# Kernel optimization log

Measured on AMD Instinct MI355X. Metric: run time of the kernel, lower is better.

The kernel has to match this reference:

```python
import jax, jax.numpy as jnp
import numpy as np

B, T, F, H, L = 128, 512, 64, 512, 2


def setup_inputs() -> dict:
    key = jax.random.key(0)
    ks = jax.random.split(key, 12)
    s = 1.0 / np.sqrt(H)
    inp = {
        "x": jax.random.normal(ks[0], (B, T, F), dtype=jnp.float32),
        "w_ih_0": jax.random.uniform(ks[1], (4 * H, F), jnp.float32, -s, s),
        "w_hh_0": jax.random.uniform(ks[2], (4 * H, H), jnp.float32, -s, s),
        "b_ih_0": jax.random.uniform(ks[3], (4 * H,), jnp.float32, -s, s),
        "b_hh_0": jax.random.uniform(ks[4], (4 * H,), jnp.float32, -s, s),
        "w_ih_1": jax.random.uniform(ks[5], (4 * H, H), jnp.float32, -s, s),
        "w_hh_1": jax.random.uniform(ks[6], (4 * H, H), jnp.float32, -s, s),
        "b_ih_1": jax.random.uniform(ks[7], (4 * H,), jnp.float32, -s, s),
        "b_hh_1": jax.random.uniform(ks[8], (4 * H,), jnp.float32, -s, s),
        "lin_w": jax.random.uniform(ks[9], (1, H), jnp.float32, -s, s),
        "lin_b": jax.random.uniform(ks[10], (1,), jnp.float32, -s, s),
    }
    return inp


def _lstm_layer(x, w_ih, w_hh, b_ih, b_hh):
    # x: [B, T, Din] -> hidden sequence [B, T, H]; PyTorch gate order i,f,g,o
    Bb = x.shape[0]
    Hh = w_hh.shape[1]
    # precompute input projections for all timesteps (big GEMM outside the scan)
    x_proj = jnp.einsum('bti,gi->btg', x, w_ih) + b_ih + b_hh  # [B, T, 4H]

    def step(carry, xt):
        h, c = carry
        gates = xt + h @ w_hh.T  # [B, 4H]
        i, f, g, o = jnp.split(gates, 4, axis=-1)
        i = jax.nn.sigmoid(i)
        f = jax.nn.sigmoid(f)
        g = jnp.tanh(g)
        o = jax.nn.sigmoid(o)
        c = f * c + i * g
        h = o * jnp.tanh(c)
        return (h, c), h

    h0 = jnp.zeros((Bb, Hh), x.dtype)
    (_, _), hs = jax.lax.scan(step, (h0, h0), jnp.swapaxes(x_proj, 0, 1))
    return jnp.swapaxes(hs, 0, 1)  # [B, T, H]


def reference(x, w_ih_0, w_hh_0, b_ih_0, b_hh_0,
              w_ih_1, w_hh_1, b_ih_1, b_hh_1, lin_w, lin_b):
    h = _lstm_layer(x, w_ih_0, w_hh_0, b_ih_0, b_hh_0)
    h = _lstm_layer(h, w_ih_1, w_hh_1, b_ih_1, b_hh_1)
    last = h[:, -1, :]           # [B, H]
    return last @ lin_w.T + lin_b  # [B, 1]
```

## Files before the change

kernel.cpp:

```cpp
#include <hip/hip_runtime.h>
#include <hip/hip_bf16.h>

typedef __bf16 bf16x8 __attribute__((ext_vector_type(8)));
typedef float f32x4 __attribute__((ext_vector_type(4)));
typedef unsigned uint4v __attribute__((ext_vector_type(4)));
typedef unsigned long long u64;

constexpr int Bb = 128, Tt = 512, Ff = 64, Hh = 512, Gg = 2048;
constexpr int K0 = Hh + Ff;
constexpr int K1 = Hh + Hh;
constexpr int NITER = Tt + 1;

constexpr size_t OFF_W0  = 0;
constexpr size_t OFF_W1  = OFF_W0 + (size_t)Gg * K0 * 2;
constexpr size_t OFF_B0  = OFF_W1 + (size_t)Gg * K1 * 2;
constexpr size_t OFF_B1  = OFF_B0 + (size_t)Gg * 4;
constexpr size_t OFF_HI0 = OFF_B1 + (size_t)Gg * 4;
constexpr size_t OFF_HI1 = OFF_HI0 + (size_t)2 * Bb * Hh * 4;
constexpr size_t OFF_HF  = OFF_HI1 + (size_t)2 * Bb * Hh * 4;
constexpr size_t OFF_FLG = OFF_HF + (size_t)Bb * Hh * 4;

__global__ void prep(const float* __restrict__ wih0, const float* __restrict__ whh0,
                     const float* __restrict__ bih0, const float* __restrict__ bhh0,
                     const float* __restrict__ wih1, const float* __restrict__ whh1,
                     const float* __restrict__ bih1, const float* __restrict__ bhh1,
                     unsigned char* __restrict__ ws)
{
  __hip_bfloat16* W0 = reinterpret_cast<__hip_bfloat16*>(ws + OFF_W0);
  __hip_bfloat16* W1 = reinterpret_cast<__hip_bfloat16*>(ws + OFF_W1);
  float* B0 = reinterpret_cast<float*>(ws + OFF_B0);
  float* B1 = reinterpret_cast<float*>(ws + OFF_B1);
  unsigned* HI0 = reinterpret_cast<unsigned*>(ws + OFF_HI0);
  unsigned* HI1 = reinterpret_cast<unsigned*>(ws + OFF_HI1);
  unsigned* FLG = reinterpret_cast<unsigned*>(ws + OFF_FLG);

  const size_t tid = (size_t)blockIdx.x * blockDim.x + threadIdx.x;
  const size_t stp = (size_t)gridDim.x * blockDim.x;

  for (size_t i = tid; i < (size_t)Gg * K0; i += stp) {
    int g = (int)(i / K0), k = (int)(i % K0);
    float v = (k < Hh) ? whh0[(size_t)g * Hh + k] : wih0[(size_t)g * Ff + (k - Hh)];
    W0[i] = __float2bfloat16(v);
  }
  for (size_t i = tid; i < (size_t)Gg * K1; i += stp) {
    int g = (int)(i / K1), k = (int)(i % K1);
    float v = (k < Hh) ? whh1[(size_t)g * Hh + k] : wih1[(size_t)g * Hh + (k - Hh)];
    W1[i] = __float2bfloat16(v);
  }
  for (size_t i = tid; i < (size_t)Gg; i += stp) {
    B0[i] = bih0[i] + bhh0[i];
    B1[i] = bih1[i] + bhh1[i];
  }
  for (size_t i = tid; i < (size_t)2 * Bb * Hh; i += stp) { HI0[i] = 0u; HI1[i] = 0u; }
  for (size_t i = tid; i < (size_t)NITER * 256; i += stp) FLG[i] = 0u;
}

__device__ __forceinline__ float sigf(float x)   { return 1.f / (1.f + __expf(-x)); }
__device__ __forceinline__ float tanhf_(float x) { return 1.f - 2.f / (1.f + __expf(2.f * x)); }

__device__ __forceinline__ unsigned pack_hl(float v) {
  __bf16 hb = (__bf16)v;
  __bf16 lb = (__bf16)(v - (float)hb);
  return (unsigned)__builtin_bit_cast(unsigned short, hb)
       | ((unsigned)__builtin_bit_cast(unsigned short, lb) << 16);
}

__device__ __forceinline__ void lds_frag(const unsigned* sh, int fr, int cb,
                                         bf16x8& hi, bf16x8& lo) {
  const int sw = (fr & 7) << 2;
  const unsigned* row = sh + fr * Hh;
  uint4v qa = *reinterpret_cast<const uint4v*>(row + (cb ^ sw));
  uint4v qb = *reinterpret_cast<const uint4v*>(row + ((cb + 4) ^ sw));
  uint4v hw = { __builtin_amdgcn_perm(qa[1], qa[0], 0x05040100u),
                __builtin_amdgcn_perm(qa[3], qa[2], 0x05040100u),
                __builtin_amdgcn_perm(qb[1], qb[0], 0x05040100u),
                __builtin_amdgcn_perm(qb[3], qb[2], 0x05040100u) };
  uint4v lw = { __builtin_amdgcn_perm(qa[1], qa[0], 0x07060302u),
                __builtin_amdgcn_perm(qa[3], qa[2], 0x07060302u),
                __builtin_amdgcn_perm(qb[1], qb[0], 0x07060302u),
                __builtin_amdgcn_perm(qb[3], qb[2], 0x07060302u) };
  hi = __builtin_bit_cast(bf16x8, hw);
  lo = __builtin_bit_cast(bf16x8, lw);
}

__device__ __forceinline__ void group_barrier(unsigned* FLG, int it, int gb, int hs,
                                              int lane, int w4) {
  asm volatile("s_waitcnt vmcnt(0)" ::: "memory");
  __syncthreads();
  unsigned* base = FLG + (size_t)it * 256 + gb * 32;
  if (threadIdx.x == 0)
    __hip_atomic_store(base + hs, 1u, __ATOMIC_RELAXED, __HIP_MEMORY_SCOPE_SYSTEM);
  if (w4 == 0 && lane < 32) {
    while (__hip_atomic_load(base + lane, __ATOMIC_RELAXED, __HIP_MEMORY_SCOPE_SYSTEM) == 0u) {}
  }
  asm volatile("" ::: "memory");
  __syncthreads();
}

__global__ __launch_bounds__(256, 1)
void lstm_main(const __hip_bfloat16* __restrict__ W0, const __hip_bfloat16* __restrict__ W1,
               const float* __restrict__ B0, const float* __restrict__ B1,
               unsigned* __restrict__ HI0, unsigned* __restrict__ HI1,
               float* __restrict__ HF, unsigned* __restrict__ FLG,
               const float* __restrict__ xg,
               const float* __restrict__ linw, const float* __restrict__ linb,
               float* __restrict__ out)
{
  const int tid  = threadIdx.x;
  const int lane = tid & 63;
  const int w4   = tid >> 6;
  const int gb   = blockIdx.x & 7;
  const int hs   = blockIdx.x >> 3;
  const int b0   = gb << 4;
  const int j0   = hs << 4;
  const int fr   = lane & 15;
  const int fk   = (lane >> 4) << 3;

  __shared__ unsigned sh0[16 * Hh];
  __shared__ unsigned sh1[16 * Hh];
  __shared__ float p0[4][4][16][20];
  __shared__ float p1[4][4][16][20];

  const int ks0 = (w4 < 2) ? w4 * 5 : 10 + (w4 - 2) * 4;
  const int kc0 = (w4 < 2) ? 5 : 4;

  bf16x8 wf0[4][5], wf1[4][8];
  #pragma unroll
  for (int g = 0; g < 4; ++g) {
    const size_t rw0 = (size_t)(g * Hh + j0 + fr) * K0;
    const size_t rw1 = (size_t)(g * Hh + j0 + fr) * K1;
    #pragma unroll
    for (int s = 0; s < 5; ++s) {
      int ks = ks0 + ((s < kc0) ? s : 0);
      wf0[g][s] = *reinterpret_cast<const bf16x8*>(W0 + rw0 + ks * 32 + fk);
    }
    #pragma unroll
    for (int s = 0; s < 8; ++s)
      wf1[g][s] = *reinterpret_cast<const bf16x8*>(W1 + rw1 + (w4 * 8 + s) * 32 + fk);
  }
  #pragma unroll
  for (int g = 0; g < 4; ++g) {
    #pragma unroll
    for (int s = 0; s < 5; ++s) asm volatile("" : "+v"(wf0[g][s]));
    #pragma unroll
    for (int s = 0; s < 8; ++s) asm volatile("" : "+v"(wf1[g][s]));
  }

  const int um = tid >> 4, uj = tid & 15;
  float bs0[4], bs1[4];
  #pragma unroll
  for (int g = 0; g < 4; ++g) {
    bs0[g] = B0[g * Hh + j0 + uj];
    bs1[g] = B1[g * Hh + j0 + uj];
  }
  float c0 = 0.f, c1 = 0.f;

  for (int it = 0; it <= Tt; ++it) {
    const int p = it & 1;
    const size_t rdo = (size_t)p * (Bb * Hh), wro = (size_t)(p ^ 1) * (Bb * Hh);

    u64 ld0[16], ld1[16];
    #pragma unroll
    for (int k = 0; k < 16; ++k)
      ld0[k] = __hip_atomic_load(
          reinterpret_cast<const u64*>(HI0 + rdo + (size_t)(b0 + k) * Hh) + tid,
          __ATOMIC_RELAXED, __HIP_MEMORY_SCOPE_SYSTEM);
    #pragma unroll
    for (int k = 0; k < 16; ++k)
      ld1[k] = __hip_atomic_load(
          reinterpret_cast<const u64*>(HI1 + rdo + (size_t)(b0 + k) * Hh) + tid,
          __ATOMIC_RELAXED, __HIP_MEMORY_SCOPE_SYSTEM);

    #pragma unroll
    for (int k = 0; k < 16; ++k) {
      const int c = (tid * 2) ^ ((k & 7) << 2);
      *reinterpret_cast<u64*>(sh0 + k * Hh + c) = ld0[k];
      *reinterpret_cast<u64*>(sh1 + k * Hh + c) = ld1[k];
    }
    __syncthreads();

    if (it < Tt) {
      bf16x8 ah[5], al[5];
      #pragma unroll
      for (int s = 0; s < 5; ++s) {
        const int k0 = (ks0 + ((s < kc0) ? s : 0)) * 32;
        if (k0 < Hh) {
          lds_frag(sh0, fr, k0 + fk, ah[s], al[s]);
        } else {
          const float* xs = xg + ((size_t)(b0 + fr) * Tt + it) * Ff + (k0 - Hh) + fk;
          f32x4 v0 = *reinterpret_cast<const f32x4*>(xs);
          f32x4 v1 = *reinterpret_cast<const f32x4*>(xs + 4);
          bf16x8 hh, ll;
          #pragma unroll
          for (int j = 0; j < 4; ++j) {
            float v = v0[j];  __bf16 hb = (__bf16)v;
            hh[j] = hb;  ll[j] = (__bf16)(v - (float)hb);
            v = v1[j];  hb = (__bf16)v;
            hh[j + 4] = hb;  ll[j + 4] = (__bf16)(v - (float)hb);
          }
          ah[s] = hh;  al[s] = ll;
        }
      }
      f32x4 acc[4] = {};
      #pragma unroll
      for (int s = 0; s < 5; ++s) {
        if (s < kc0) {
          #pragma unroll
          for (int g = 0; g < 4; ++g) {
            acc[g] = __builtin_amdgcn_mfma_f32_16x16x32_bf16(ah[s], wf0[g][s], acc[g], 0, 0, 0);
            acc[g] = __builtin_amdgcn_mfma_f32_16x16x32_bf16(al[s], wf0[g][s], acc[g], 0, 0, 0);
          }
        }
      }
      #pragma unroll
      for (int g = 0; g < 4; ++g)
        *reinterpret_cast<f32x4*>(&p0[w4][g][fr][(lane >> 4) << 2]) = acc[g];
    }

    if (it >= 1) {
      f32x4 acc[4] = {};
      #pragma unroll
      for (int s = 0; s < 8; ++s) {
        const int k0 = (w4 * 8 + s) * 32;
        bf16x8 ah, al;
        if (k0 < Hh) lds_frag(sh1, fr, k0 + fk, ah, al);
        else         lds_frag(sh0, fr, (k0 - Hh) + fk, ah, al);
        #pragma unroll
        for (int g = 0; g < 4; ++g) {
          acc[g] = __builtin_amdgcn_mfma_f32_16x16x32_bf16(ah, wf1[g][s], acc[g], 0, 0, 0);
          acc[g] = __builtin_amdgcn_mfma_f32_16x16x32_bf16(al, wf1[g][s], acc[g], 0, 0, 0);
        }
      }
      #pragma unroll
      for (int g = 0; g < 4; ++g)
        *reinterpret_cast<f32x4*>(&p1[w4][g][fr][(lane >> 4) << 2]) = acc[g];
    }
    __syncthreads();

    if (it < Tt) {
      float gv[4];
      #pragma unroll
      for (int g = 0; g < 4; ++g)
        gv[g] = p0[0][g][uj][um] + p0[1][g][uj][um] + p0[2][g][uj][um] + p0[3][g][uj][um] + bs0[g];
      float iv = sigf(gv[0]), fv = sigf(gv[1]), gg = tanhf_(gv[2]), ov = sigf(gv[3]);
      c0 = fv * c0 + iv * gg;
      float hv = ov * tanhf_(c0);
      __hip_atomic_store(HI0 + wro + (size_t)(b0 + um) * Hh + j0 + uj, pack_hl(hv),
                         __ATOMIC_RELAXED, __HIP_MEMORY_SCOPE_SYSTEM);
    }
    if (it >= 1) {
      float gv[4];
      #pragma unroll
      for (int g = 0; g < 4; ++g)
        gv[g] = p1[0][g][uj][um] + p1[1][g][uj][um] + p1[2][g][uj][um] + p1[3][g][uj][um] + bs1[g];
      float iv = sigf(gv[0]), fv = sigf(gv[1]), gg = tanhf_(gv[2]), ov = sigf(gv[3]);
      c1 = fv * c1 + iv * gg;
      float hv = ov * tanhf_(c1);
      __hip_atomic_store(HI1 + wro + (size_t)(b0 + um) * Hh + j0 + uj, pack_hl(hv),
                         __ATOMIC_RELAXED, __HIP_MEMORY_SCOPE_SYSTEM);
      if (it == Tt)
        __hip_atomic_store(HF + (size_t)(b0 + um) * Hh + j0 + uj, hv,
                           __ATOMIC_RELAXED, __HIP_MEMORY_SCOPE_SYSTEM);
    }

    group_barrier(FLG, it, gb, hs, lane, w4);
  }

  if (hs < 16 && tid < 64) {
    const int b = (gb << 4) + hs;
    float s = 0.f;
    #pragma unroll
    for (int i = 0; i < 8; ++i) {
      int j = i * 64 + tid;
      float hv = __hip_atomic_load(HF + (size_t)b * Hh + j, __ATOMIC_RELAXED,
                                   __HIP_MEMORY_SCOPE_SYSTEM);
      s += hv * linw[j];
    }
    #pragma unroll
    for (int off = 32; off >= 1; off >>= 1) s += __shfl_down(s, off, 64);
    if (tid == 0) out[b] = s + linb[0];
  }
}

extern "C" void kernel_launch(void* const* d_in, const int* in_sizes, int n_in,
                              void* d_out, int out_size, void* d_ws, size_t ws_size,
                              hipStream_t stream)
{
  const float* x    = (const float*)d_in[0];
  const float* wih0 = (const float*)d_in[1];
  const float* whh0 = (const float*)d_in[2];
  const float* bih0 = (const float*)d_in[3];
  const float* bhh0 = (const float*)d_in[4];
  const float* wih1 = (const float*)d_in[5];
  const float* whh1 = (const float*)d_in[6];
  const float* bih1 = (const float*)d_in[7];
  const float* bhh1 = (const float*)d_in[8];
  const float* linw = (const float*)d_in[9];
  const float* linb = (const float*)d_in[10];
  float* outp = (float*)d_out;
  unsigned char* ws = (unsigned char*)d_ws;

  prep<<<256, 256, 0, stream>>>(wih0, whh0, bih0, bhh0, wih1, whh1, bih1, bhh1, ws);

  lstm_main<<<256, 256, 0, stream>>>(
      (const __hip_bfloat16*)(ws + OFF_W0), (const __hip_bfloat16*)(ws + OFF_W1),
      (const float*)(ws + OFF_B0), (const float*)(ws + OFF_B1),
      (unsigned*)(ws + OFF_HI0), (unsigned*)(ws + OFF_HI1),
      (float*)(ws + OFF_HF), (unsigned*)(ws + OFF_FLG),
      x, linw, linb, outp);
}
```

Baseline: 2.834 ms.

## Split per-step group barrier into separate layer-0 and layer-1 flag waits

Replaces the single end-of-iteration group barrier with two separate flag sets, one per LSTM layer. Each layer publishes its own completion flag right after writing its hidden state and waits only on the flag it actually depends on. The layer-0 gate computation now runs before the layer-1 MFMA work, so layer-0 results are published earlier. The x-input conversion is also hoisted to the start of the iteration. This is meant to let layer-0 progress overlap with layer-1 compute across blocks, at the cost of more barriers and flag traffic, with the flag array doubled in size.

```diff
diff --git a/kernel.cpp b/kernel.cpp
--- a/kernel.cpp
+++ b/kernel.cpp
@@ -7,7 +7,7 @@
 typedef unsigned long long u64;
 
 constexpr int Bb = 128, Tt = 512, Ff = 64, Hh = 512, Gg = 2048;
-constexpr int K0 = Hh + Ff;
+constexpr int K0 = Hh + 64;
 constexpr int K1 = Hh + Hh;
 constexpr int NITER = Tt + 1;
 
@@ -39,7 +39,7 @@
 
   for (size_t i = tid; i < (size_t)Gg * K0; i += stp) {
     int g = (int)(i / K0), k = (int)(i % K0);
-    float v = (k < Hh) ? whh0[(size_t)g * Hh + k] : wih0[(size_t)g * Ff + (k - Hh)];
+    float v = (k < Hh) ? whh0[(size_t)g * Hh + k] : wih0[(size_t)g * 64 + (k - Hh)];
     W0[i] = __float2bfloat16(v);
   }
   for (size_t i = tid; i < (size_t)Gg * K1; i += stp) {
@@ -52,7 +52,7 @@
     B1[i] = bih1[i] + bhh1[i];
   }
   for (size_t i = tid; i < (size_t)2 * Bb * Hh; i += stp) { HI0[i] = 0u; HI1[i] = 0u; }
-  for (size_t i = tid; i < (size_t)NITER * 256; i += stp) FLG[i] = 0u;
+  for (size_t i = tid; i < (size_t)NITER * 512; i += stp) FLG[i] = 0u;
 }
 
 __device__ __forceinline__ float sigf(float x)   { return 1.f / (1.f + __expf(-x)); }
@@ -83,18 +83,19 @@
   lo = __builtin_bit_cast(bf16x8, lw);
 }
 
-__device__ __forceinline__ void group_barrier(unsigned* FLG, int it, int gb, int hs,
-                                              int lane, int w4) {
+__device__ __forceinline__ void wait_flags(const unsigned* base, int lane, int w4) {
+  if (w4 == 0 && lane < 32) {
+    while (__hip_atomic_load(base + lane, __ATOMIC_RELAXED, __HIP_MEMORY_SCOPE_SYSTEM) == 0u) {}
+  }
+  asm volatile("" ::: "memory");
+  __syncthreads();
+}
+
+__device__ __forceinline__ void set_flag(unsigned* slot, int hs) {
   asm volatile("s_waitcnt vmcnt(0)" ::: "memory");
   __syncthreads();
-  unsigned* base = FLG + (size_t)it * 256 + gb * 32;
   if (threadIdx.x == 0)
-    __hip_atomic_store(base + hs, 1u, __ATOMIC_RELAXED, __HIP_MEMORY_SCOPE_SYSTEM);
-  if (w4 == 0 && lane < 32) {
-    while (__hip_atomic_load(base + lane, __ATOMIC_RELAXED, __HIP_MEMORY_SCOPE_SYSTEM) == 0u) {}
-  }
-  asm volatile("" ::: "memory");
-  __syncthreads();
+    __hip_atomic_store(slot, 1u, __ATOMIC_RELAXED, __HIP_MEMORY_SCOPE_SYSTEM);
 }
 
 __global__ __launch_bounds__(256, 1)
@@ -159,12 +160,36 @@
     const int p = it & 1;
     const size_t rdo = (size_t)p * (Bb * Hh), wro = (size_t)(p ^ 1) * (Bb * Hh);
 
-    u64 ld0[16], ld1[16];
+    bf16x8 axh0{}, axl0{}, axh1{}, axl1{};
+    if (w4 == 3 && it < Tt) {
+      const float* xr = xg + ((size_t)(b0 + fr) * Tt + it) * 64 + fk;
+      #pragma unroll
+      for (int s2 = 0; s2 < 2; ++s2) {
+        f32x4 v0 = *reinterpret_cast<const f32x4*>(xr + s2 * 32);
+        f32x4 v1 = *reinterpret_cast<const f32x4*>(xr + s2 * 32 + 4);
+        bf16x8 hh, ll;
+        #pragma unroll
+        for (int j = 0; j < 4; ++j) {
+          float v = v0[j];  __bf16 hb = (__bf16)v;
+          hh[j] = hb;  ll[j] = (__bf16)(v - (float)hb);
+          v = v1[j];  hb = (__bf16)v;
+          hh[j + 4] = hb;  ll[j + 4] = (__bf16)(v - (float)hb);
+        }
+        if (s2 == 0) { axh0 = hh; axl0 = ll; } else { axh1 = hh; axl1 = ll; }
+      }
+    }
+
+    if (it >= 1)
+      wait_flags(FLG + ((size_t)(it - 1) * 2 + 0) * 256 + gb * 32, lane, w4);
+    u64 ld0[16];
     #pragma unroll
     for (int k = 0; k < 16; ++k)
       ld0[k] = __hip_atomic_load(
           reinterpret_cast<const u64*>(HI0 + rdo + (size_t)(b0 + k) * Hh) + tid,
           __ATOMIC_RELAXED, __HIP_MEMORY_SCOPE_SYSTEM);
+    if (it >= 2)
+      wait_flags(FLG + ((size_t)(it - 2) * 2 + 1) * 256 + gb * 32, lane, w4);
+    u64 ld1[16];
     #pragma unroll
     for (int k = 0; k < 16; ++k)
       ld1[k] = __hip_atomic_load(
@@ -172,33 +197,21 @@
           __ATOMIC_RELAXED, __HIP_MEMORY_SCOPE_SYSTEM);
 
     #pragma unroll
-    for (int k = 0; k < 16; ++k) {
-      const int c = (tid * 2) ^ ((k & 7) << 2);
-      *reinterpret_cast<u64*>(sh0 + k * Hh + c) = ld0[k];
-      *reinterpret_cast<u64*>(sh1 + k * Hh + c) = ld1[k];
-    }
+    for (int k = 0; k < 16; ++k)
+      *reinterpret_cast<u64*>(sh0 + k * Hh + ((tid * 2) ^ ((k & 7) << 2))) = ld0[k];
     __syncthreads();
 
     if (it < Tt) {
       bf16x8 ah[5], al[5];
       #pragma unroll
       for (int s = 0; s < 5; ++s) {
-        const int k0 = (ks0 + ((s < kc0) ? s : 0)) * 32;
+        const int ks = ks0 + ((s < kc0) ? s : 0);
+        const int k0 = ks * 32;
         if (k0 < Hh) {
           lds_frag(sh0, fr, k0 + fk, ah[s], al[s]);
         } else {
-          const float* xs = xg + ((size_t)(b0 + fr) * Tt + it) * Ff + (k0 - Hh) + fk;
-          f32x4 v0 = *reinterpret_cast<const f32x4*>(xs);
-          f32x4 v1 = *reinterpret_cast<const f32x4*>(xs + 4);
-          bf16x8 hh, ll;
-          #pragma unroll
-          for (int j = 0; j < 4; ++j) {
-            float v = v0[j];  __bf16 hb = (__bf16)v;
-            hh[j] = hb;  ll[j] = (__bf16)(v - (float)hb);
-            v = v1[j];  hb = (__bf16)v;
-            hh[j + 4] = hb;  ll[j + 4] = (__bf16)(v - (float)hb);
-          }
-          ah[s] = hh;  al[s] = ll;
+          ah[s] = (ks == 16) ? axh0 : axh1;
+          al[s] = (ks == 16) ? axl0 : axl1;
         }
       }
       f32x4 acc[4] = {};
@@ -215,6 +228,25 @@
       #pragma unroll
       for (int g = 0; g < 4; ++g)
         *reinterpret_cast<f32x4*>(&p0[w4][g][fr][(lane >> 4) << 2]) = acc[g];
+    }
+    __syncthreads();
+
+    #pragma unroll
+    for (int k = 0; k < 16; ++k)
+      *reinterpret_cast<u64*>(sh1 + k * Hh + ((tid * 2) ^ ((k & 7) << 2))) = ld1[k];
+    if (it < Tt) {
+      float gv[4];
+      #pragma unroll
+      for (int g = 0; g < 4; ++g)
+        gv[g] = p0[0][g][uj][um] + p0[1][g][uj][um] + p0[2][g][uj][um] + p0[3][g][uj][um] + bs0[g];
+      float iv = sigf(gv[0]), fv = sigf(gv[1]), gg = tanhf_(gv[2]), ov = sigf(gv[3]);
+      c0 = fv * c0 + iv * gg;
+      float hv = ov * tanhf_(c0);
+      __hip_atomic_store(HI0 + wro + (size_t)(b0 + um) * Hh + j0 + uj, pack_hl(hv),
+                         __ATOMIC_RELAXED, __HIP_MEMORY_SCOPE_SYSTEM);
+      set_flag(FLG + ((size_t)it * 2 + 0) * 256 + gb * 32 + hs, hs);
+    } else {
+      __syncthreads();
     }
 
     if (it >= 1) {
@@ -237,17 +269,6 @@
     }
     __syncthreads();
 
-    if (it < Tt) {
-      float gv[4];
-      #pragma unroll
-      for (int g = 0; g < 4; ++g)
-        gv[g] = p0[0][g][uj][um] + p0[1][g][uj][um] + p0[2][g][uj][um] + p0[3][g][uj][um] + bs0[g];
-      float iv = sigf(gv[0]), fv = sigf(gv[1]), gg = tanhf_(gv[2]), ov = sigf(gv[3]);
-      c0 = fv * c0 + iv * gg;
-      float hv = ov * tanhf_(c0);
-      __hip_atomic_store(HI0 + wro + (size_t)(b0 + um) * Hh + j0 + uj, pack_hl(hv),
-                         __ATOMIC_RELAXED, __HIP_MEMORY_SCOPE_SYSTEM);
-    }
     if (it >= 1) {
       float gv[4];
       #pragma unroll
@@ -261,10 +282,11 @@
       if (it == Tt)
         __hip_atomic_store(HF + (size_t)(b0 + um) * Hh + j0 + uj, hv,
                            __ATOMIC_RELAXED, __HIP_MEMORY_SCOPE_SYSTEM);
-    }
-
-    group_barrier(FLG, it, gb, hs, lane, w4);
-  }
+      set_flag(FLG + ((size_t)(it - 1) * 2 + 1) * 256 + gb * 32 + hs, hs);
+    }
+  }
+
+  wait_flags(FLG + ((size_t)(Tt - 1) * 2 + 1) * 256 + gb * 32, lane, w4);
 
   if (hs < 16 && tid < 64) {
     const int b = (gb << 4) + hs;
```

After: 2.885 ms. No clear change (+1.8%).
